# Kernel tuning notes

Measured on AMD Instinct MI355X. Metric: run time of the kernel, lower is better.

## Reference

```python
import jax, jax.numpy as jnp
import numpy as np

B, N, D, H, W, OUT = 2, 2048, 128, 8, 4, 256

def setup_inputs() -> dict:
    key = jax.random.key(0)
    ks = jax.random.split(key, 8)
    s = 0.02
    return {
        "nodefeatures": jax.random.normal(ks[0], (B, N, D), jnp.float32),
        "nodeadj": jax.random.uniform(ks[1], (B, N, N, W), jnp.float32),
        "Wq": jax.random.normal(ks[2], (H, D, D), jnp.float32) * s,
        "bq": jnp.zeros((H, D), jnp.float32),
        "Wk": jax.random.normal(ks[3], (H, D, D), jnp.float32) * s,
        "bk": jnp.zeros((H, D), jnp.float32),
        "Wv": jax.random.normal(ks[4], (H, D, D), jnp.float32) * s,
        "bv": jnp.zeros((H, D), jnp.float32),
        "Wout": jax.random.normal(ks[5], (H * D, OUT), jnp.float32) * s,
        "bout": jnp.zeros((OUT,), jnp.float32),
    }

def reference(nodefeatures, nodeadj, Wq, bq, Wk, bk, Wv, bv, Wout, bout):
    # Per-head linear projections, all heads at once: [B,H,N,D]
    q = jnp.einsum('bnd,hde->bhne', nodefeatures, Wq) + bq[None, :, None, :]
    k = jnp.einsum('bnd,hde->bhne', nodefeatures, Wk) + bk[None, :, None, :]
    v = jnp.einsum('bnd,hde->bhne', nodefeatures, Wv) + bv[None, :, None, :]
    # Original scales by k.shape[1]**0.5 == sqrt(N) (node count, not head dim)
    scores = jnp.einsum('bhnd,bhmd->bhnm', q, k) / jnp.sqrt(jnp.asarray(N, q.dtype))
    # (scores[...,None] * nodeadj).sum(-1) == scores * nodeadj.sum(-1)
    scores = scores * nodeadj.sum(-1)[:, None, :, :]  # [B,H,N,N]
    attn = jax.nn.softmax(scores, axis=-1)  # torch softmax(dim=2) on [B,N,N] == key axis
    o = jnp.einsum('bhnm,bhmd->bhnd', attn, v)
    o = jnp.moveaxis(o, 1, 2).reshape(B, N, H * D)  # concat heads along feature dim
    return o @ Wout + bout
```

## Files before the change

### kernel.cpp

```cpp
#include <hip/hip_runtime.h>
#include <hip/hip_bf16.h>

#define BB 2
#define NN 2048
#define DD 128
#define HH 8
#define OUTD 256
#define SCALE 0.022097086912079612f

typedef __bf16 bf16x8 __attribute__((ext_vector_type(8)));
typedef float f32x4 __attribute__((ext_vector_type(4)));
typedef _Float16 f16x4 __attribute__((ext_vector_type(4)));

__device__ __forceinline__ unsigned short f2bf(float f) {
    union { float f; unsigned int u; } v; v.f = f;
    unsigned int r = (v.u + 0x7FFFu + ((v.u >> 16) & 1u)) >> 16;
    return (unsigned short)r;
}
__device__ __forceinline__ float bf2f(unsigned short s) {
    union { unsigned int u; float f; } v; v.u = ((unsigned int)s) << 16;
    return v.f;
}
__device__ __forceinline__ void gl_lds16(const unsigned short* g, unsigned short* l) {
    __builtin_amdgcn_global_load_lds(
        (const __attribute__((address_space(1))) unsigned int*)g,
        (__attribute__((address_space(3))) unsigned int*)l,
        16, 0, 0);
}

__global__ __launch_bounds__(256) void prep_kernel(
    const float* __restrict__ X,
    const float* __restrict__ Wq,
    const float* __restrict__ Wk,
    const float* __restrict__ Wv,
    const float* __restrict__ Wout,
    unsigned short* __restrict__ Xb,
    unsigned short* __restrict__ WT,
    unsigned short* __restrict__ WoutT)
{
    __shared__ unsigned short T[128 * 136];
    const int bid = blockIdx.x;
    const int t = threadIdx.x;

    if (bid < 512) {
        int i4 = (bid * 256 + t) * 4;
        float4 v = *(const float4*)(X + i4);
        unsigned short u[4] = {f2bf(v.x), f2bf(v.y), f2bf(v.z), f2bf(v.w)};
        *(ushort4*)(Xb + i4) = *(const ushort4*)u;
    } else if (bid < 536) {
        const int mh = bid - 512;
        const int mat = mh >> 3, h = mh & 7;
        const float* Wm = (mat == 0) ? Wq : ((mat == 1) ? Wk : Wv);
        Wm += (size_t)h * DD * DD;
        #pragma unroll
        for (int i = 0; i < 16; ++i) {
            int lin = i * 256 + t;
            int d = lin >> 5, e = (lin & 31) * 4;
            float4 v = *(const float4*)(Wm + (size_t)d * DD + e);
            unsigned short u[4] = {f2bf(v.x), f2bf(v.y), f2bf(v.z), f2bf(v.w)};
            *(uint2*)&T[d * 136 + e] = *(const uint2*)u;
        }
        __syncthreads();
        const int e = t >> 1, nh = t & 1;
        unsigned short* Wo = WT + ((size_t)mat * HH + h) * (DD * DD) + (size_t)e * DD + nh * 64;
        #pragma unroll
        for (int j = 0; j < 8; ++j) {
            unsigned short tmp[8];
            #pragma unroll
            for (int k = 0; k < 8; ++k)
                tmp[k] = T[(nh * 64 + j * 8 + k) * 136 + e];
            *(uint4*)(Wo + j * 8) = *(const uint4*)tmp;
        }
    } else {
        const int kb = bid - 536;
        #pragma unroll
        for (int i = 0; i < 16; ++i) {
            int lin = i * 256 + t;
            int k = lin >> 6, o = (lin & 63) * 4;
            float4 v = *(const float4*)(Wout + (size_t)(kb * 64 + k) * OUTD + o);
            unsigned short u[4] = {f2bf(v.x), f2bf(v.y), f2bf(v.z), f2bf(v.w)};
            *(uint2*)&T[k * 264 + o] = *(const uint2*)u;
        }
        __syncthreads();
        unsigned short* Wo = WoutT + (size_t)t * (HH * DD) + kb * 64;
        #pragma unroll
        for (int j = 0; j < 8; ++j) {
            unsigned short tmp[8];
            #pragma unroll
            for (int k = 0; k < 8; ++k)
                tmp[k] = T[(j * 8 + k) * 264 + t];
            *(uint4*)(Wo + j * 8) = *(const uint4*)tmp;
        }
    }
}

__global__ void adjsum_kernel(const float4* __restrict__ adj, unsigned short* __restrict__ s) {
    int idx = blockIdx.x * blockDim.x + threadIdx.x;
    float4 a = adj[idx];
    s[idx] = f2bf((a.x + a.y) + (a.z + a.w));
}

__global__ __launch_bounds__(256) void proj_kernel(
    const unsigned short* __restrict__ Xb,
    const unsigned short* __restrict__ WT,
    const float* __restrict__ bq, const float* __restrict__ bk, const float* __restrict__ bv,
    unsigned short* __restrict__ Qo, unsigned short* __restrict__ Ko,
    unsigned short* __restrict__ Vt)
{
    const int mat = blockIdx.z;
    const int bh  = blockIdx.y;
    const int b = bh >> 3, h = bh & 7;
    const int n0 = blockIdx.x * 64;
    const int tid = threadIdx.x;
    const int lane = tid & 63, wv = tid >> 6;
    const int m = lane & 15, quad = lane >> 4;

    __shared__ unsigned short Wlds[128 * 136];

    const unsigned short* Wg = WT + ((size_t)mat * HH + h) * (DD * DD);
    #pragma unroll
    for (int i = tid; i < 128 * 16; i += 256) {
        int r = i >> 4, c = i & 15;
        *(uint4*)&Wlds[r * 136 + c * 8] = *(const uint4*)(Wg + r * 128 + c * 8);
    }

    const int row = n0 + wv * 16 + m;
    const unsigned short* Xr = Xb + ((size_t)b * NN + row) * DD;
    bf16x8 af[4];
    #pragma unroll
    for (int kc = 0; kc < 4; ++kc)
        af[kc] = *(const bf16x8*)(Xr + kc * 32 + quad * 8);

    __syncthreads();

    f32x4 acc[8];
    #pragma unroll
    for (int et = 0; et < 8; ++et) acc[et] = (f32x4){0.f, 0.f, 0.f, 0.f};

    #pragma unroll
    for (int kc = 0; kc < 4; ++kc) {
        #pragma unroll
        for (int et = 0; et < 8; ++et) {
            bf16x8 bfrg = *(const bf16x8*)&Wlds[(et * 16 + m) * 136 + kc * 32 + quad * 8];
            acc[et] = __builtin_amdgcn_mfma_f32_16x16x32_bf16(af[kc], bfrg, acc[et], 0, 0, 0);
        }
    }

    const float* bias = (mat == 0) ? bq : ((mat == 1) ? bk : bv);
    if (mat != 2) {
        #pragma unroll
        for (int et = 0; et < 8; ++et) {
            int e = et * 16 + m;
            float bb = bias[h * DD + e];
            #pragma unroll
            for (int reg = 0; reg < 4; ++reg) {
                int r = n0 + wv * 16 + quad * 4 + reg;
                unsigned short v16 = f2bf(acc[et][reg] + bb);
                if (mat == 0) Qo[((size_t)bh * NN + r) * DD + e] = v16;
                else          Ko[((size_t)bh * NN + r) * DD + e] = v16;
            }
        }
    } else {
        __syncthreads();
        #pragma unroll
        for (int et = 0; et < 8; ++et) {
            int e = et * 16 + m;
            float bb = bias[h * DD + e];
            #pragma unroll
            for (int reg = 0; reg < 4; ++reg)
                Wlds[(wv * 16 + quad * 4 + reg) * 136 + e] = f2bf(acc[et][reg] + bb);
        }
        __syncthreads();
        const int e = tid >> 1, nh = tid & 1;
        #pragma unroll
        for (int j = 0; j < 4; ++j) {
            unsigned short tmp[8];
            #pragma unroll
            for (int kk = 0; kk < 8; ++kk)
                tmp[kk] = Wlds[(nh * 32 + j * 8 + kk) * 136 + e];
            *(uint4*)(Vt + ((size_t)bh * DD + e) * NN + n0 + nh * 32 + j * 8) = *(uint4*)tmp;
        }
    }
}

__global__ __launch_bounds__(256, 2) void attn_kernel(
    const unsigned short* __restrict__ Q,
    const unsigned short* __restrict__ K,
    const unsigned short* __restrict__ Vt,
    const unsigned short* __restrict__ adjs,
    _Float16* __restrict__ Opart,
    float* __restrict__ Lpart)
{
    const int L = blockIdx.x;
    const int xcd = L & 7, W = L >> 3;
    const int b  = (xcd >> 2) & 1;
    const int ks = (xcd >> 1) & 1;
    const int h  = (xcd & 1) * 4 + (W & 3);
    const int qt = W >> 2;
    const int bh = b * HH + h;
    const int q0 = qt * 128;
    const int kstart = ks * 1024;
    const int tid = threadIdx.x;
    const int lane = tid & 63, wv = tid >> 6;
    const int m = lane & 15, quad = lane >> 4;

    __shared__ unsigned short Kb[2][32 * 128];
    __shared__ unsigned short Vb[2][128 * 32];
    __shared__ unsigned short Plds[4][2][16 * 40];

    const unsigned short* Kbase = K + (size_t)bh * NN * DD;
    const unsigned short* Vbase = Vt + (size_t)bh * DD * NN;

    bf16x8 qf[2][4];
    #pragma unroll
    for (int qg = 0; qg < 2; ++qg) {
        const unsigned short* Qr = Q + ((size_t)bh * NN + q0 + wv * 32 + qg * 16 + m) * DD;
        #pragma unroll
        for (int kc = 0; kc < 4; ++kc)
            qf[qg][kc] = *(const bf16x8*)(Qr + kc * 32 + quad * 8);
    }

    f32x4 o[2][8];
    #pragma unroll
    for (int qg = 0; qg < 2; ++qg)
        #pragma unroll
        for (int dt = 0; dt < 8; ++dt) o[qg][dt] = (f32x4){0.f, 0.f, 0.f, 0.f};
    float li[2][4] = {{0.f,0.f,0.f,0.f},{0.f,0.f,0.f,0.f}};

    const unsigned short* Abase = adjs + ((size_t)b * NN + q0 + wv * 32 + quad * 4) * NN;

    const int kr4 = lane >> 4, kc16 = lane & 15;
    const int vr16 = lane >> 2, vc4 = lane & 3;

    #define STAGE(buf, kbase_)                                                              \
        {                                                                                   \
            _Pragma("unroll")                                                               \
            for (int j2 = 0; j2 < 2; ++j2) {                                                \
                const int j = wv * 2 + j2;                                                  \
                const int krow = j * 4 + kr4;                                               \
                gl_lds16(Kbase + (size_t)((kbase_) + krow) * DD + ((kc16 ^ (krow & 15)) * 8),\
                         &Kb[buf][j * 512]);                                                \
                const int vrow = j * 16 + vr16;                                             \
                gl_lds16(Vbase + (size_t)vrow * NN + (kbase_) + ((vc4 ^ ((vr16 >> 1) & 3)) * 8),\
                         &Vb[buf][j * 512]);                                                \
            }                                                                               \
        }

    STAGE(0, kstart);
    __syncthreads();

    for (int kt = 0; kt < 32; ++kt) {
        const int cb = kt & 1, nb = cb ^ 1;
        const int k0 = kstart + kt * 32;

        float areg[2][2][4];
        #pragma unroll
        for (int qg = 0; qg < 2; ++qg)
            #pragma unroll
            for (int nt = 0; nt < 2; ++nt)
                #pragma unroll
                for (int reg = 0; reg < 4; ++reg)
                    areg[qg][nt][reg] =
                        bf2f(Abase[(size_t)(qg * 16 + reg) * NN + k0 + nt * 16 + m]) * SCALE;

        if (kt + 1 < 32) STAGE(nb, k0 + 32);

        f32x4 s[2][2];
        s[0][0] = (f32x4){0.f,0.f,0.f,0.f}; s[0][1] = (f32x4){0.f,0.f,0.f,0.f};
        s[1][0] = (f32x4){0.f,0.f,0.f,0.f}; s[1][1] = (f32x4){0.f,0.f,0.f,0.f};
        #pragma unroll
        for (int kc = 0; kc < 4; ++kc) {
            #pragma unroll
            for (int nt = 0; nt < 2; ++nt) {
                bf16x8 kf = *(const bf16x8*)&Kb[cb][(nt * 16 + m) * 128 + (((kc * 4 + quad) ^ m) * 8)];
                s[0][nt] = __builtin_amdgcn_mfma_f32_16x16x32_bf16(qf[0][kc], kf, s[0][nt], 0, 0, 0);
                s[1][nt] = __builtin_amdgcn_mfma_f32_16x16x32_bf16(qf[1][kc], kf, s[1][nt], 0, 0, 0);
            }
        }

        #pragma unroll
        for (int qg = 0; qg < 2; ++qg)
            #pragma unroll
            for (int nt = 0; nt < 2; ++nt)
                #pragma unroll
                for (int reg = 0; reg < 4; ++reg) {
                    float p = __expf(s[qg][nt][reg] * areg[qg][nt][reg]);
                    li[qg][reg] += p;
                    Plds[wv][qg][(quad * 4 + reg) * 40 + nt * 16 + m] = f2bf(p);
                }

        bf16x8 pf0 = *(const bf16x8*)&Plds[wv][0][m * 40 + quad * 8];
        bf16x8 pf1 = *(const bf16x8*)&Plds[wv][1][m * 40 + quad * 8];
        #pragma unroll
        for (int dt = 0; dt < 8; ++dt) {
            bf16x8 vf = *(const bf16x8*)&Vb[cb][(dt * 16 + m) * 32 + ((quad ^ ((m >> 1) & 3)) * 8)];
            o[0][dt] = __builtin_amdgcn_mfma_f32_16x16x32_bf16(pf0, vf, o[0][dt], 0, 0, 0);
            o[1][dt] = __builtin_amdgcn_mfma_f32_16x16x32_bf16(pf1, vf, o[1][dt], 0, 0, 0);
        }

        __syncthreads();
    }
    #undef STAGE

    #pragma unroll
    for (int qg = 0; qg < 2; ++qg) {
        #pragma unroll
        for (int reg = 0; reg < 4; ++reg) {
            float t = li[qg][reg];
            t += __shfl_xor(t, 1);
            t += __shfl_xor(t, 2);
            t += __shfl_xor(t, 4);
            t += __shfl_xor(t, 8);
            li[qg][reg] = t;
        }
        const int rbase = q0 + wv * 32 + qg * 16 + quad * 4;
        if (m == 0) {
            #pragma unroll
            for (int reg = 0; reg < 4; ++reg)
                Lpart[((size_t)ks * (BB * HH) + bh) * NN + rbase + reg] = li[qg][reg];
        }
        #pragma unroll
        for (int reg = 0; reg < 4; ++reg) {
            const size_t obase = (((size_t)ks * (BB * HH) + bh) * NN + rbase + reg) * DD;
            #pragma unroll
            for (int dt = 0; dt < 8; ++dt)
                Opart[obase + dt * 16 + m] = (_Float16)o[qg][dt][reg];
        }
    }
}

__global__ void combine_kernel(const _Float16* __restrict__ Op,
                               const float* __restrict__ Lp,
                               unsigned short* __restrict__ Ocat)
{
    const int SPLIT_OFF = BB * HH * NN * DD;
    int t = blockIdx.x * blockDim.x + threadIdx.x;
    int e0 = t * 4;
    int row = e0 >> 7;
    float l = 1.0f / (Lp[row] + Lp[row + BB * HH * NN]);
    f16x4 a = *(const f16x4*)(Op + e0);
    f16x4 c = *(const f16x4*)(Op + SPLIT_OFF + e0);
    int bh = row >> 11, n = row & (NN - 1);
    int b = bh >> 3, h = bh & 7;
    size_t obase = ((size_t)(b * NN + n)) * (HH * DD) + h * DD + (e0 & (DD - 1));
    unsigned short u[4];
    #pragma unroll
    for (int i = 0; i < 4; ++i)
        u[i] = f2bf(((float)a[i] + (float)c[i]) * l);
    *(ushort4*)(Ocat + obase) = *(ushort4*)u;
}

__global__ __launch_bounds__(256) void out_kernel(
    const unsigned short* __restrict__ Ocat,
    const unsigned short* __restrict__ WoutT,
    const float* __restrict__ bout,
    float* __restrict__ out)
{
    const int m0 = blockIdx.x * 32;
    const int c0 = blockIdx.y * 64;
    const int tid = threadIdx.x;
    const int lane = tid & 63, wv = tid >> 6;
    const int m = lane & 15, quad = lane >> 4;
    const int mg = wv & 1, cg = wv >> 1;

    __shared__ unsigned short Wlds[64 * 136];

    f32x4 acc[2];
    acc[0] = (f32x4){0.f,0.f,0.f,0.f};
    acc[1] = (f32x4){0.f,0.f,0.f,0.f};

    const unsigned short* Orow = Ocat + (size_t)(m0 + mg * 16 + m) * (HH * DD);

    for (int kc = 0; kc < 8; ++kc) {
        #pragma unroll
        for (int i = tid; i < 64 * 16; i += 256) {
            int rr = i >> 4, c = i & 15;
            *(uint4*)&Wlds[rr * 136 + c * 8] =
                *(const uint4*)(WoutT + (size_t)(c0 + rr) * (HH * DD) + kc * 128 + c * 8);
        }
        __syncthreads();
        #pragma unroll
        for (int j = 0; j < 4; ++j) {
            bf16x8 afr = *(const bf16x8*)(Orow + kc * 128 + j * 32 + quad * 8);
            #pragma unroll
            for (int nt = 0; nt < 2; ++nt) {
                bf16x8 bfr = *(const bf16x8*)&Wlds[(cg * 32 + nt * 16 + m) * 136 + j * 32 + quad * 8];
                acc[nt] = __builtin_amdgcn_mfma_f32_16x16x32_bf16(afr, bfr, acc[nt], 0, 0, 0);
            }
        }
        __syncthreads();
    }

    #pragma unroll
    for (int nt = 0; nt < 2; ++nt) {
        int oc = c0 + cg * 32 + nt * 16 + m;
        float bb = bout[oc];
        #pragma unroll
        for (int reg = 0; reg < 4; ++reg) {
            int rr = m0 + mg * 16 + quad * 4 + reg;
            out[(size_t)rr * OUTD + oc] = acc[nt][reg] + bb;
        }
    }
}

extern "C" void kernel_launch(void* const* d_in, const int* in_sizes, int n_in,
                              void* d_out, int out_size, void* d_ws, size_t ws_size,
                              hipStream_t stream)
{
    const float* X    = (const float*)d_in[0];
    const float* adj  = (const float*)d_in[1];
    const float* Wq   = (const float*)d_in[2];
    const float* bq   = (const float*)d_in[3];
    const float* Wk   = (const float*)d_in[4];
    const float* bk   = (const float*)d_in[5];
    const float* Wv   = (const float*)d_in[6];
    const float* bv   = (const float*)d_in[7];
    const float* Wout = (const float*)d_in[8];
    const float* bout = (const float*)d_in[9];
    float* out = (float*)d_out;

    char* ws = (char*)d_ws;
    unsigned short* Xb    = (unsigned short*)(ws);
    unsigned short* WT    = (unsigned short*)(ws + 1048576);
    unsigned short* WoutT = (unsigned short*)(ws + 1835008);
    unsigned short* Q     = (unsigned short*)(ws + 2359296);
    unsigned short* Kp    = (unsigned short*)(ws + 10747904);
    unsigned short* Vt    = (unsigned short*)(ws + 19136512);
    unsigned short* AsumB = (unsigned short*)(ws + 27525120);
    _Float16*       Opart = (_Float16*)(ws + 44302336);
    unsigned short* Ocat  = (unsigned short*)(ws + 61079552);
    float*          Lpart = (float*)(ws);

    prep_kernel<<<552, 256, 0, stream>>>(X, Wq, Wk, Wv, Wout, Xb, WT, WoutT);
    adjsum_kernel<<<(BB * NN * NN) / 256, 256, 0, stream>>>((const float4*)adj, AsumB);
    proj_kernel<<<dim3(NN / 64, BB * HH, 3), 256, 0, stream>>>(Xb, WT, bq, bk, bv, Q, Kp, Vt);
    attn_kernel<<<512, 256, 0, stream>>>(Q, Kp, Vt, AsumB, Opart, Lpart);
    combine_kernel<<<(BB * HH * NN * DD / 4) / 256, 256, 0, stream>>>(Opart, Lpart, Ocat);
    out_kernel<<<dim3((BB * NN) / 32, OUTD / 64), 256, 0, stream>>>(Ocat, WoutT, bout, out);
}
```

Before: 312.6 us.

## Fuse adjacency sum into prep, split keys three ways, fold combine into output GEMM

The adjacency sum moves into the prep kernel, which now writes a transposed, pre-scaled (including log2e) bf16 matrix. The attention kernel stages that matrix tile-wise into LDS with swizzled async loads instead of doing strided scalar global reads. The key range is split three ways instead of two (768 blocks, 3 blocks per CU). P and V switch to fp16 MFMA, with exp2 replacing expf. The separate combine kernel is removed: the output GEMM sums the three partials and normalizes on the fly in fp16. This cuts kernel launches and global traffic, at the risk of fp16 range and precision issues in P·V and in the output GEMM inputs.

After: 326.3 us. +4.4%, slower.

```diff
diff --git a/kernel.cpp b/kernel.cpp
--- a/kernel.cpp
+++ b/kernel.cpp
@@ -5,12 +5,13 @@
 #define NN 2048
 #define DD 128
 #define HH 8
+#define HD 1024
 #define OUTD 256
-#define SCALE 0.022097086912079612f
+#define ASCALE 0.031879357f
 
 typedef __bf16 bf16x8 __attribute__((ext_vector_type(8)));
 typedef float f32x4 __attribute__((ext_vector_type(4)));
-typedef _Float16 f16x4 __attribute__((ext_vector_type(4)));
+typedef _Float16 f16x8 __attribute__((ext_vector_type(8)));
 
 __device__ __forceinline__ unsigned short f2bf(float f) {
     union { float f; unsigned int u; } v; v.f = f;
@@ -21,7 +22,12 @@
     union { unsigned int u; float f; } v; v.u = ((unsigned int)s) << 16;
     return v.f;
 }
-__device__ __forceinline__ void gl_lds16(const unsigned short* g, unsigned short* l) {
+__device__ __forceinline__ unsigned short f2h_bits(float f) {
+    _Float16 h = (_Float16)f;
+    union { _Float16 h; unsigned short u; } v; v.h = h;
+    return v.u;
+}
+__device__ __forceinline__ void gl_lds16(const void* g, void* l) {
     __builtin_amdgcn_global_load_lds(
         (const __attribute__((address_space(1))) unsigned int*)g,
         (__attribute__((address_space(3))) unsigned int*)l,
@@ -30,25 +36,41 @@
 
 __global__ __launch_bounds__(256) void prep_kernel(
     const float* __restrict__ X,
+    const float4* __restrict__ adj,
     const float* __restrict__ Wq,
     const float* __restrict__ Wk,
     const float* __restrict__ Wv,
     const float* __restrict__ Wout,
     unsigned short* __restrict__ Xb,
     unsigned short* __restrict__ WT,
-    unsigned short* __restrict__ WoutT)
+    unsigned short* __restrict__ WoutT,
+    unsigned short* __restrict__ AsumT)
 {
     __shared__ unsigned short T[128 * 136];
     const int bid = blockIdx.x;
     const int t = threadIdx.x;
 
-    if (bid < 512) {
-        int i4 = (bid * 256 + t) * 4;
+    if (bid < 4096) {
+        const int b = bid >> 11, rem = bid & 2047;
+        const int q0 = (rem >> 6) * 64, k0 = (rem & 63) * 32;
+        const int q_l = t >> 2, kg = t & 3;
+        const float4* arow = adj + ((size_t)(b * NN + q0 + q_l)) * NN + k0 + kg * 8;
+        #pragma unroll
+        for (int j = 0; j < 8; ++j) {
+            float4 v = arow[j];
+            T[(kg * 8 + j) * 68 + q_l] = f2bf(((v.x + v.y) + (v.z + v.w)) * ASCALE);
+        }
+        __syncthreads();
+        const int key = t >> 3, ch = t & 7;
+        *(uint4*)&AsumT[(size_t)(b * NN + k0 + key) * NN + q0 + ch * 8] =
+            *(const uint4*)&T[key * 68 + ch * 8];
+    } else if (bid < 4608) {
+        int i4 = ((bid - 4096) * 256 + t) * 4;
         float4 v = *(const float4*)(X + i4);
         unsigned short u[4] = {f2bf(v.x), f2bf(v.y), f2bf(v.z), f2bf(v.w)};
         *(ushort4*)(Xb + i4) = *(const ushort4*)u;
-    } else if (bid < 536) {
-        const int mh = bid - 512;
+    } else if (bid < 4632) {
+        const int mh = bid - 4608;
         const int mat = mh >> 3, h = mh & 7;
         const float* Wm = (mat == 0) ? Wq : ((mat == 1) ? Wk : Wv);
         Wm += (size_t)h * DD * DD;
@@ -72,17 +94,17 @@
             *(uint4*)(Wo + j * 8) = *(const uint4*)tmp;
         }
     } else {
-        const int kb = bid - 536;
+        const int kb = bid - 4632;
         #pragma unroll
         for (int i = 0; i < 16; ++i) {
             int lin = i * 256 + t;
             int k = lin >> 6, o = (lin & 63) * 4;
             float4 v = *(const float4*)(Wout + (size_t)(kb * 64 + k) * OUTD + o);
-            unsigned short u[4] = {f2bf(v.x), f2bf(v.y), f2bf(v.z), f2bf(v.w)};
+            unsigned short u[4] = {f2h_bits(v.x), f2h_bits(v.y), f2h_bits(v.z), f2h_bits(v.w)};
             *(uint2*)&T[k * 264 + o] = *(const uint2*)u;
         }
         __syncthreads();
-        unsigned short* Wo = WoutT + (size_t)t * (HH * DD) + kb * 64;
+        unsigned short* Wo = WoutT + (size_t)t * HD + kb * 64;
         #pragma unroll
         for (int j = 0; j < 8; ++j) {
             unsigned short tmp[8];
@@ -92,12 +114,6 @@
             *(uint4*)(Wo + j * 8) = *(const uint4*)tmp;
         }
     }
-}
-
-__global__ void adjsum_kernel(const float4* __restrict__ adj, unsigned short* __restrict__ s) {
-    int idx = blockIdx.x * blockDim.x + threadIdx.x;
-    float4 a = adj[idx];
-    s[idx] = f2bf((a.x + a.y) + (a.z + a.w));
 }
 
 __global__ __launch_bounds__(256) void proj_kernel(
@@ -168,7 +184,7 @@
             float bb = bias[h * DD + e];
             #pragma unroll
             for (int reg = 0; reg < 4; ++reg)
-                Wlds[(wv * 16 + quad * 4 + reg) * 136 + e] = f2bf(acc[et][reg] + bb);
+                Wlds[(wv * 16 + quad * 4 + reg) * 136 + e] = f2h_bits(acc[et][reg] + bb);
         }
         __syncthreads();
         const int e = tid >> 1, nh = tid & 1;
@@ -183,33 +199,34 @@
     }
 }
 
-__global__ __launch_bounds__(256, 2) void attn_kernel(
+__global__ __launch_bounds__(256, 3) void attn_kernel(
     const unsigned short* __restrict__ Q,
     const unsigned short* __restrict__ K,
     const unsigned short* __restrict__ Vt,
-    const unsigned short* __restrict__ adjs,
+    const unsigned short* __restrict__ AsumT,
     _Float16* __restrict__ Opart,
     float* __restrict__ Lpart)
 {
     const int L = blockIdx.x;
-    const int xcd = L & 7, W = L >> 3;
-    const int b  = (xcd >> 2) & 1;
-    const int ks = (xcd >> 1) & 1;
-    const int h  = (xcd & 1) * 4 + (W & 3);
-    const int qt = W >> 2;
+    const int ks = L % 3;
+    const int t1 = L / 3;
+    const int qt = t1 & 15, h = (t1 >> 4) & 7, b = t1 >> 7;
     const int bh = b * HH + h;
     const int q0 = qt * 128;
-    const int kstart = ks * 1024;
+    const int kstart = (ks == 0) ? 0 : (704 + (ks - 1) * 672);
+    const int nkt = (ks == 0) ? 22 : 21;
     const int tid = threadIdx.x;
     const int lane = tid & 63, wv = tid >> 6;
     const int m = lane & 15, quad = lane >> 4;
 
     __shared__ unsigned short Kb[2][32 * 128];
     __shared__ unsigned short Vb[2][128 * 32];
-    __shared__ unsigned short Plds[4][2][16 * 40];
+    __shared__ unsigned short Ab[32 * 128];
+    __shared__ _Float16 Plds[4][2][16 * 40];
 
     const unsigned short* Kbase = K + (size_t)bh * NN * DD;
     const unsigned short* Vbase = Vt + (size_t)bh * DD * NN;
+    const unsigned short* ATb   = AsumT + (size_t)b * NN * NN;
 
     bf16x8 qf[2][4];
     #pragma unroll
@@ -227,12 +244,11 @@
         for (int dt = 0; dt < 8; ++dt) o[qg][dt] = (f32x4){0.f, 0.f, 0.f, 0.f};
     float li[2][4] = {{0.f,0.f,0.f,0.f},{0.f,0.f,0.f,0.f}};
 
-    const unsigned short* Abase = adjs + ((size_t)b * NN + q0 + wv * 32 + quad * 4) * NN;
-
     const int kr4 = lane >> 4, kc16 = lane & 15;
     const int vr16 = lane >> 2, vc4 = lane & 3;
-
-    #define STAGE(buf, kbase_)                                                              \
+    const int akey4 = lane >> 4, aqc = lane & 15;
+
+    #define STAGE_KV(buf, kbase_)                                                          \
         {                                                                                   \
             _Pragma("unroll")                                                               \
             for (int j2 = 0; j2 < 2; ++j2) {                                                \
@@ -245,25 +261,41 @@
                          &Vb[buf][j * 512]);                                                \
             }                                                                               \
         }
-
-    STAGE(0, kstart);
+    #define STAGE_A(kbase_)                                                                 \
+        {                                                                                   \
+            _Pragma("unroll")                                                               \
+            for (int j2 = 0; j2 < 2; ++j2) {                                                \
+                const int key = wv * 8 + j2 * 4 + akey4;                                    \
+                gl_lds16(ATb + (size_t)((kbase_) + key) * NN + q0 + ((aqc ^ (key & 15)) * 8),\
+                         &Ab[(wv * 8 + j2 * 4) * 128]);                                     \
+            }                                                                               \
+        }
+
+    STAGE_KV(0, kstart);
+    STAGE_A(kstart);
     __syncthreads();
 
-    for (int kt = 0; kt < 32; ++kt) {
+    for (int kt = 0; kt < nkt; ++kt) {
         const int cb = kt & 1, nb = cb ^ 1;
         const int k0 = kstart + kt * 32;
 
         float areg[2][2][4];
         #pragma unroll
-        for (int qg = 0; qg < 2; ++qg)
-            #pragma unroll
-            for (int nt = 0; nt < 2; ++nt)
-                #pragma unroll
-                for (int reg = 0; reg < 4; ++reg)
-                    areg[qg][nt][reg] =
-                        bf2f(Abase[(size_t)(qg * 16 + reg) * NN + k0 + nt * 16 + m]) * SCALE;
-
-        if (kt + 1 < 32) STAGE(nb, k0 + 32);
+        for (int qg = 0; qg < 2; ++qg) {
+            const int qlc = wv * 4 + qg * 2 + (quad >> 1);
+            #pragma unroll
+            for (int nt = 0; nt < 2; ++nt) {
+                ushort4 av = *(const ushort4*)&Ab[(nt * 16 + m) * 128 +
+                                                  ((qlc ^ m) * 8) + (quad & 1) * 4];
+                areg[qg][nt][0] = bf2f(av.x);
+                areg[qg][nt][1] = bf2f(av.y);
+                areg[qg][nt][2] = bf2f(av.z);
+                areg[qg][nt][3] = bf2f(av.w);
+            }
+        }
+        __syncthreads();
+
+        if (kt + 1 < nkt) { STAGE_KV(nb, k0 + 32); STAGE_A(k0 + 32); }
 
         f32x4 s[2][2];
         s[0][0] = (f32x4){0.f,0.f,0.f,0.f}; s[0][1] = (f32x4){0.f,0.f,0.f,0.f};
@@ -284,23 +316,24 @@
             for (int nt = 0; nt < 2; ++nt)
                 #pragma unroll
                 for (int reg = 0; reg < 4; ++reg) {
-                    float p = __expf(s[qg][nt][reg] * areg[qg][nt][reg]);
+                    float p = exp2f(s[qg][nt][reg] * areg[qg][nt][reg]);
                     li[qg][reg] += p;
-                    Plds[wv][qg][(quad * 4 + reg) * 40 + nt * 16 + m] = f2bf(p);
+                    Plds[wv][qg][(quad * 4 + reg) * 40 + nt * 16 + m] = (_Float16)p;
                 }
 
-        bf16x8 pf0 = *(const bf16x8*)&Plds[wv][0][m * 40 + quad * 8];
-        bf16x8 pf1 = *(const bf16x8*)&Plds[wv][1][m * 40 + quad * 8];
+        f16x8 pf0 = *(const f16x8*)&Plds[wv][0][m * 40 + quad * 8];
+        f16x8 pf1 = *(const f16x8*)&Plds[wv][1][m * 40 + quad * 8];
         #pragma unroll
         for (int dt = 0; dt < 8; ++dt) {
-            bf16x8 vf = *(const bf16x8*)&Vb[cb][(dt * 16 + m) * 32 + ((quad ^ ((m >> 1) & 3)) * 8)];
-            o[0][dt] = __builtin_amdgcn_mfma_f32_16x16x32_bf16(pf0, vf, o[0][dt], 0, 0, 0);
-            o[1][dt] = __builtin_amdgcn_mfma_f32_16x16x32_bf16(pf1, vf, o[1][dt], 0, 0, 0);
-        }
-
-        __syncthreads();
-    }
-    #undef STAGE
+            f16x8 vf = *(const f16x8*)&Vb[cb][(dt * 16 + m) * 32 + ((quad ^ ((m >> 1) & 3)) * 8)];
+            o[0][dt] = __builtin_amdgcn_mfma_f32_16x16x32_f16(pf0, vf, o[0][dt], 0, 0, 0);
+            o[1][dt] = __builtin_amdgcn_mfma_f32_16x16x32_f16(pf1, vf, o[1][dt], 0, 0, 0);
+        }
+
+        __syncthreads();
+    }
+    #undef STAGE_KV
+    #undef STAGE_A
 
     #pragma unroll
     for (int qg = 0; qg < 2; ++qg) {
@@ -317,11 +350,11 @@
         if (m == 0) {
             #pragma unroll
             for (int reg = 0; reg < 4; ++reg)
-                Lpart[((size_t)ks * (BB * HH) + bh) * NN + rbase + reg] = li[qg][reg];
+                Lpart[(size_t)(ks * BB * NN + b * NN + rbase + reg) * HH + h] = li[qg][reg];
         }
         #pragma unroll
         for (int reg = 0; reg < 4; ++reg) {
-            const size_t obase = (((size_t)ks * (BB * HH) + bh) * NN + rbase + reg) * DD;
+            const size_t obase = (size_t)(ks * BB * NN + b * NN + rbase + reg) * HD + h * DD;
             #pragma unroll
             for (int dt = 0; dt < 8; ++dt)
                 Opart[obase + dt * 16 + m] = (_Float16)o[qg][dt][reg];
@@ -329,33 +362,15 @@
     }
 }
 
-__global__ void combine_kernel(const _Float16* __restrict__ Op,
-                               const float* __restrict__ Lp,
-                               unsigned short* __restrict__ Ocat)
-{
-    const int SPLIT_OFF = BB * HH * NN * DD;
-    int t = blockIdx.x * blockDim.x + threadIdx.x;
-    int e0 = t * 4;
-    int row = e0 >> 7;
-    float l = 1.0f / (Lp[row] + Lp[row + BB * HH * NN]);
-    f16x4 a = *(const f16x4*)(Op + e0);
-    f16x4 c = *(const f16x4*)(Op + SPLIT_OFF + e0);
-    int bh = row >> 11, n = row & (NN - 1);
-    int b = bh >> 3, h = bh & 7;
-    size_t obase = ((size_t)(b * NN + n)) * (HH * DD) + h * DD + (e0 & (DD - 1));
-    unsigned short u[4];
-    #pragma unroll
-    for (int i = 0; i < 4; ++i)
-        u[i] = f2bf(((float)a[i] + (float)c[i]) * l);
-    *(ushort4*)(Ocat + obase) = *(ushort4*)u;
-}
-
 __global__ __launch_bounds__(256) void out_kernel(
-    const unsigned short* __restrict__ Ocat,
+    const _Float16* __restrict__ Op,
+    const float* __restrict__ Lp,
     const unsigned short* __restrict__ WoutT,
     const float* __restrict__ bout,
     float* __restrict__ out)
 {
+    const int OFFS = BB * NN * HD;
+    const int LOFF = BB * NN * HH;
     const int m0 = blockIdx.x * 32;
     const int c0 = blockIdx.y * 64;
     const int tid = threadIdx.x;
@@ -364,28 +379,46 @@
     const int mg = wv & 1, cg = wv >> 1;
 
     __shared__ unsigned short Wlds[64 * 136];
+    __shared__ float Llds[32 * 8];
+
+    {
+        const int rl = tid >> 3, hh = tid & 7;
+        const int ri = m0 + rl;
+        float l = Lp[(size_t)ri * HH + hh] + Lp[(size_t)(LOFF + ri * HH) + hh] +
+                  Lp[(size_t)(2 * LOFF + ri * HH) + hh];
+        Llds[rl * 8 + hh] = 1.0f / l;
+    }
 
     f32x4 acc[2];
     acc[0] = (f32x4){0.f,0.f,0.f,0.f};
     acc[1] = (f32x4){0.f,0.f,0.f,0.f};
 
-    const unsigned short* Orow = Ocat + (size_t)(m0 + mg * 16 + m) * (HH * DD);
+    const int row_l = mg * 16 + m;
+    const size_t ri = (size_t)(m0 + row_l);
 
     for (int kc = 0; kc < 8; ++kc) {
         #pragma unroll
         for (int i = tid; i < 64 * 16; i += 256) {
             int rr = i >> 4, c = i & 15;
             *(uint4*)&Wlds[rr * 136 + c * 8] =
-                *(const uint4*)(WoutT + (size_t)(c0 + rr) * (HH * DD) + kc * 128 + c * 8);
-        }
-        __syncthreads();
+                *(const uint4*)(WoutT + (size_t)(c0 + rr) * HD + kc * 128 + c * 8);
+        }
+        __syncthreads();
+        _Float16 hl = (_Float16)Llds[row_l * 8 + kc];
+        f16x8 hlv;
+        #pragma unroll
+        for (int i = 0; i < 8; ++i) hlv[i] = hl;
         #pragma unroll
         for (int j = 0; j < 4; ++j) {
-            bf16x8 afr = *(const bf16x8*)(Orow + kc * 128 + j * 32 + quad * 8);
+            const size_t abase = ri * HD + kc * 128 + j * 32 + quad * 8;
+            f16x8 a0 = *(const f16x8*)(Op + abase);
+            f16x8 a1 = *(const f16x8*)(Op + OFFS + abase);
+            f16x8 a2 = *(const f16x8*)(Op + 2 * (size_t)OFFS + abase);
+            f16x8 afr = ((a0 + a1) + a2) * hlv;
             #pragma unroll
             for (int nt = 0; nt < 2; ++nt) {
-                bf16x8 bfr = *(const bf16x8*)&Wlds[(cg * 32 + nt * 16 + m) * 136 + j * 32 + quad * 8];
-                acc[nt] = __builtin_amdgcn_mfma_f32_16x16x32_bf16(afr, bfr, acc[nt], 0, 0, 0);
+                f16x8 bfr = *(const f16x8*)&Wlds[(cg * 32 + nt * 16 + m) * 136 + j * 32 + quad * 8];
+                acc[nt] = __builtin_amdgcn_mfma_f32_16x16x32_f16(afr, bfr, acc[nt], 0, 0, 0);
             }
         }
         __syncthreads();
@@ -426,15 +459,13 @@
     unsigned short* Q     = (unsigned short*)(ws + 2359296);
     unsigned short* Kp    = (unsigned short*)(ws + 10747904);
     unsigned short* Vt    = (unsigned short*)(ws + 19136512);
-    unsigned short* AsumB = (unsigned short*)(ws + 27525120);
+    unsigned short* AsumT = (unsigned short*)(ws + 27525120);
     _Float16*       Opart = (_Float16*)(ws + 44302336);
-    unsigned short* Ocat  = (unsigned short*)(ws + 61079552);
     float*          Lpart = (float*)(ws);
 
-    prep_kernel<<<552, 256, 0, stream>>>(X, Wq, Wk, Wv, Wout, Xb, WT, WoutT);
-    adjsum_kernel<<<(BB * NN * NN) / 256, 256, 0, stream>>>((const float4*)adj, AsumB);
+    prep_kernel<<<4648, 256, 0, stream>>>(X, (const float4*)adj, Wq, Wk, Wv, Wout,
+                                          Xb, WT, WoutT, AsumT);
     proj_kernel<<<dim3(NN / 64, BB * HH, 3), 256, 0, stream>>>(Xb, WT, bq, bk, bv, Q, Kp, Vt);
-    attn_kernel<<<512, 256, 0, stream>>>(Q, Kp, Vt, AsumB, Opart, Lpart);
-    combine_kernel<<<(BB * HH * NN * DD / 4) / 256, 256, 0, stream>>>(Opart, Lpart, Ocat);
-    out_kernel<<<dim3((BB * NN) / 32, OUTD / 64), 256, 0, stream>>>(Ocat, WoutT, bout, out);
-}
+    attn_kernel<<<768, 256, 0, stream>>>(Q, Kp, Vt, AsumT, Opart, Lpart);
+    out_kernel<<<dim3((BB * NN) / 32, OUTD / 64), 256, 0, stream>>>(Opart, Lpart, WoutT, bout, out);
+}
```
